# Optimization experiments

Measured on AMD Instinct MI355X. Metric: run time of the kernel, lower is better.

Reference implementation:

```python
import jax, jax.numpy as jnp
import numpy as np

D_MODEL = 256
N_HEADS = 8
D_FF = 1024
N_LAYERS = 6
INPUT_DIM = 2
EPS = 1e-5  # torch LayerNorm default


def _layer_norm(x, g, b):
    m = jnp.mean(x, axis=-1, keepdims=True)
    v = jnp.mean((x - m) ** 2, axis=-1, keepdims=True)
    return (x - m) / jnp.sqrt(v + EPS) * g + b


def setup_inputs() -> dict:
    key = jax.random.key(0)
    ks = jax.random.split(key, 8)
    f32 = jnp.float32

    def w(k, shape, fan_in):
        return jax.random.normal(k, shape, f32) * (1.0 / np.sqrt(fan_in))

    return {
        "x": jax.random.normal(ks[0], (8, 1024, INPUT_DIM), f32),
        "in_w": w(ks[1], (INPUT_DIM, D_MODEL), INPUT_DIM),
        "in_b": jnp.zeros((D_MODEL,), f32),
        "ln1_g": jnp.ones((D_MODEL,), f32),
        "ln1_b": jnp.zeros((D_MODEL,), f32),
        "qkv_w": w(ks[2], (D_MODEL, 3 * D_MODEL), D_MODEL),
        "qkv_b": jnp.zeros((3 * D_MODEL,), f32),
        "out_w": w(ks[3], (D_MODEL, D_MODEL), D_MODEL),
        "out_b": jnp.zeros((D_MODEL,), f32),
        "lna_g": jnp.ones((D_MODEL,), f32),
        "lna_b": jnp.zeros((D_MODEL,), f32),
        "ln2_g": jnp.ones((D_MODEL,), f32),
        "ln2_b": jnp.zeros((D_MODEL,), f32),
        "ff1_w": w(ks[4], (D_MODEL, D_FF), D_MODEL),
        "ff1_b": jnp.zeros((D_FF,), f32),
        "ff2_w": w(ks[5], (D_FF, D_MODEL), D_FF),
        "ff2_b": jnp.zeros((D_MODEL,), f32),
        "lnf_g": jnp.ones((D_MODEL,), f32),
        "lnf_b": jnp.zeros((D_MODEL,), f32),
    }


def reference(x, in_w, in_b, ln1_g, ln1_b, qkv_w, qkv_b, out_w, out_b,
              lna_g, lna_b, ln2_g, ln2_b, ff1_w, ff1_b, ff2_w, ff2_b,
              lnf_g, lnf_b):
    B, L, _ = x.shape
    dk = D_MODEL // N_HEADS
    scale = 1.0 / np.sqrt(dk)
    top_k = max(1, L // 4)

    # sinusoidal positional encoding [L, D]
    pos = jnp.arange(L, dtype=jnp.float32)[:, None]
    div = jnp.exp(jnp.arange(0, D_MODEL, 2, dtype=jnp.float32)
                  * (-np.log(10000.0) / D_MODEL))
    pe = jnp.zeros((L, D_MODEL), jnp.float32)
    pe = pe.at[:, 0::2].set(jnp.sin(pos * div))
    pe = pe.at[:, 1::2].set(jnp.cos(pos * div))

    h = x @ in_w + in_b + pe[None]  # [B, L, D]

    # VoformerEncoder reuses the SAME layer object -> shared weights, 6 passes
    for _ in range(N_LAYERS):
        # --- self-attention sublayer (pre-norm) ---
        s2 = _layer_norm(h, ln1_g, ln1_b)
        qkv = (s2 @ qkv_w + qkv_b).reshape(B, L, 3, N_HEADS, dk)
        q = qkv[:, :, 0].transpose(0, 2, 1, 3)  # [B, H, L, dk]
        k = qkv[:, :, 1].transpose(0, 2, 1, 3)
        v = qkv[:, :, 2].transpose(0, 2, 1, 3)

        scores = jnp.einsum('bhqd,bhkd->bhqk', q, k) * scale  # [B,H,L,L]
        # ProbSparse: keep only the per-row top-k scores
        thr = jax.lax.top_k(scores, top_k)[0][..., -1:]
        sparse = jnp.where(scores >= thr, scores, -jnp.inf)
        attn = jax.nn.softmax(sparse, axis=-1)
        o = jnp.einsum('bhqk,bhkd->bhqd', attn, v)
        o = o.transpose(0, 2, 1, 3).reshape(B, L, D_MODEL)
        o = o @ out_w + out_b
        # InformerAttention applies its own residual + LayerNorm
        attn_out = _layer_norm(o + s2, lna_g, lna_b)
        h = h + attn_out

        # --- FFN sublayer with Volatilite activation ---
        s2 = _layer_norm(h, ln2_g, ln2_b)
        f = s2 @ ff1_w + ff1_b  # [B, L, d_ff]
        mean_f = jnp.mean(f, axis=1, keepdims=True)
        vol = jnp.sqrt(jnp.mean((mean_f - f) ** 2, axis=1, keepdims=True))
        f = f * vol
        f = f @ ff2_w + ff2_b
        h = h + f

    return _layer_norm(h, lnf_g, lnf_b)
```

## Files before the change

kernel.cpp:

```cpp
#include <hip/hip_runtime.h>
#include <math.h>

#define D_MODEL 256
#define NH 8
#define DFF 1024
#define NLAYERS 6
#define B_ 8
#define L_ 1024
#define NR (B_*L_)
#define TOPK 256
#define LNEPS 1e-5f

typedef __attribute__((ext_vector_type(8))) short bf16x8;
typedef __attribute__((ext_vector_type(4))) float f32x4;

__device__ __forceinline__ float wsum(float v){
  #pragma unroll
  for(int o=32;o>0;o>>=1) v += __shfl_xor(v,o,64);
  return v;
}
__device__ __forceinline__ short f2bf(float x){
  unsigned u = __float_as_uint(x);
  u += 0x7fffu + ((u>>16)&1u);
  return (short)(u>>16);
}
__device__ __forceinline__ float bf2f(short s){
  return __uint_as_float(((unsigned)(unsigned short)s)<<16);
}
__device__ __forceinline__ int sortkey(unsigned u){
  return (u & 0x8000u) ? (int)(u ^ 0xFFFFu) : (int)(u | 0x8000u);
}
__device__ __forceinline__ float kinvf(int k){
  unsigned u = (k & 0x8000) ? ((unsigned)k ^ 0x8000u) : ((unsigned)k ^ 0xFFFFu);
  return __uint_as_float(u << 16);
}
__device__ __forceinline__ void g2l(const short* g, short* l){
  __builtin_amdgcn_global_load_lds(
      (const __attribute__((address_space(1))) unsigned int*)g,
      (__attribute__((address_space(3))) unsigned int*)l,
      16, 0, 0);
}

__global__ __launch_bounds__(256) void embed_kernel(
    const float* __restrict__ x, const float* __restrict__ in_w,
    const float* __restrict__ in_b, float* __restrict__ h)
{
  int tid = blockIdx.x*256 + threadIdx.x;
  int n  = tid >> 6;
  int d0 = (tid & 63) << 2;
  int l  = n & (L_-1);
  float x0 = x[2*n], x1 = x[2*n+1];
  const float kf = -0.07195578415606394f;
  float pe[4];
  #pragma unroll
  for(int ii=0; ii<2; ++ii){
    int i = (d0>>1) + ii;
    float dv  = expf((float)i * kf);
    float ang = (float)l * dv;
    pe[2*ii]   = sinf(ang);
    pe[2*ii+1] = cosf(ang);
  }
  float4 w0 = *(const float4*)(in_w + d0);
  float4 w1 = *(const float4*)(in_w + D_MODEL + d0);
  float4 bb = *(const float4*)(in_b + d0);
  float4 o;
  o.x = x0*w0.x + x1*w1.x + bb.x + pe[0];
  o.y = x0*w0.y + x1*w1.y + bb.y + pe[1];
  o.z = x0*w0.z + x1*w1.z + bb.z + pe[2];
  o.w = x0*w0.w + x1*w1.w + bb.w + pe[3];
  *(float4*)(h + (size_t)n*D_MODEL + d0) = o;
}

__global__ __launch_bounds__(256) void wcvt(
    const float* __restrict__ W, short* __restrict__ WT, int N, int kshift)
{
  int idx = blockIdx.x*256 + threadIdx.x;
  int K = 1<<kshift;
  if (idx >= N*K) return;
  int n = idx >> kshift, k = idx & (K-1);
  WT[idx] = f2bf(W[(size_t)k*N + n]);
}

template<int OM>
__global__ __launch_bounds__(256) void ln_kernel(
    const float* __restrict__ in, const float* __restrict__ g,
    const float* __restrict__ b, float* __restrict__ out,
    short* __restrict__ outb)
{
  int wave = threadIdx.x >> 6, lane = threadIdx.x & 63;
  int row = blockIdx.x*4 + wave;
  float4 v = ((const float4*)(in + (size_t)row*D_MODEL))[lane];
  float s  = v.x+v.y+v.z+v.w;
  float sq = v.x*v.x+v.y*v.y+v.z*v.z+v.w*v.w;
  s = wsum(s); sq = wsum(sq);
  float mean = s*(1.f/D_MODEL);
  float var  = sq*(1.f/D_MODEL) - mean*mean;
  float rstd = 1.f/sqrtf(var + LNEPS);
  float4 gv = ((const float4*)g)[lane];
  float4 bv = ((const float4*)b)[lane];
  float4 o;
  o.x = (v.x-mean)*rstd*gv.x + bv.x;
  o.y = (v.y-mean)*rstd*gv.y + bv.y;
  o.z = (v.z-mean)*rstd*gv.z + bv.z;
  o.w = (v.w-mean)*rstd*gv.w + bv.w;
  if (OM == 0){
    ((float4*)(out + (size_t)row*D_MODEL))[lane] = o;
  }
  if (OM == 2){
    short4 s4; s4.x=f2bf(o.x); s4.y=f2bf(o.y); s4.z=f2bf(o.z); s4.w=f2bf(o.w);
    *(short4*)(outb + (size_t)row*D_MODEL + lane*4) = s4;
  }
}

__global__ __launch_bounds__(256) void lnln_kernel(
    const float* __restrict__ tb,
    const float* __restrict__ ga, const float* __restrict__ ba,
    const float* __restrict__ g2, const float* __restrict__ b2,
    float* __restrict__ h, short* __restrict__ s2b)
{
  int wave = threadIdx.x >> 6, lane = threadIdx.x & 63;
  int row = blockIdx.x*4 + wave;
  float4 v = ((const float4*)(tb + (size_t)row*D_MODEL))[lane];
  float s  = v.x+v.y+v.z+v.w;
  float sq = v.x*v.x+v.y*v.y+v.z*v.z+v.w*v.w;
  s = wsum(s); sq = wsum(sq);
  float mean = s*(1.f/D_MODEL);
  float var  = sq*(1.f/D_MODEL) - mean*mean;
  float rstd = 1.f/sqrtf(var + LNEPS);
  float4 gv = ((const float4*)ga)[lane];
  float4 bv = ((const float4*)ba)[lane];
  float4* hp = (float4*)(h + (size_t)row*D_MODEL) + lane;
  float4 hv = *hp;
  float4 hn;
  hn.x = hv.x + (v.x-mean)*rstd*gv.x + bv.x;
  hn.y = hv.y + (v.y-mean)*rstd*gv.y + bv.y;
  hn.z = hv.z + (v.z-mean)*rstd*gv.z + bv.z;
  hn.w = hv.w + (v.w-mean)*rstd*gv.w + bv.w;
  *hp = hn;
  float s2  = hn.x+hn.y+hn.z+hn.w;
  float sq2 = hn.x*hn.x+hn.y*hn.y+hn.z*hn.z+hn.w*hn.w;
  s2 = wsum(s2); sq2 = wsum(sq2);
  float m2 = s2*(1.f/D_MODEL);
  float v2 = sq2*(1.f/D_MODEL) - m2*m2;
  float r2 = 1.f/sqrtf(v2 + LNEPS);
  float4 g2v = ((const float4*)g2)[lane];
  float4 b2v = ((const float4*)b2)[lane];
  short4 s4;
  s4.x = f2bf((hn.x-m2)*r2*g2v.x + b2v.x);
  s4.y = f2bf((hn.y-m2)*r2*g2v.y + b2v.y);
  s4.z = f2bf((hn.z-m2)*r2*g2v.z + b2v.z);
  s4.w = f2bf((hn.w-m2)*r2*g2v.w + b2v.w);
  *(short4*)(s2b + (size_t)row*D_MODEL + lane*4) = s4;
}

template<int MODE>
__global__ __launch_bounds__(256) void mfma_gemm(
    const short* __restrict__ A, const short* __restrict__ BT,
    const float* __restrict__ bias, const short* __restrict__ residb,
    float* __restrict__ Cf, short* __restrict__ Cb, short* __restrict__ Vt,
    int N, int K)
{
  __shared__ __align__(16) short As[128*32];
  __shared__ __align__(16) short Bs[64*32];
  const int t = threadIdx.x, wv = t>>6, lane = t&63;
  const int r16 = lane&15, quad = lane>>4;
  const int m0 = blockIdx.y*128, n0 = blockIdx.x*64;
  const int ia0 = wv*128 + lane, ia1 = ia0 + 64;
  const int ib  = wv*64 + lane;
  const short* Ab = A  + (size_t)m0*K;
  const short* Bb = BT + (size_t)n0*K;
  const f32x4 z = {0.f,0.f,0.f,0.f};
  f32x4 acc[2][4];
  #pragma unroll
  for (int i=0;i<2;++i)
    #pragma unroll
    for (int j=0;j<4;++j) acc[i][j] = z;

  for (int k0 = 0; k0 < K; k0 += 32){
    __syncthreads();
    g2l(Ab + (size_t)(ia0>>2)*K + k0 + (ia0&3)*8, As + ia0*8);
    g2l(Ab + (size_t)(ia1>>2)*K + k0 + (ia1&3)*8, As + ia1*8);
    g2l(Bb + (size_t)(ib>>2)*K  + k0 + (ib&3)*8,  Bs + ib*8);
    __syncthreads();
    bf16x8 af0 = *(const bf16x8*)(As + ((wv*32      + r16)*32 + quad*8));
    bf16x8 af1 = *(const bf16x8*)(As + ((wv*32 + 16 + r16)*32 + quad*8));
    bf16x8 bf[4];
    #pragma unroll
    for (int ct=0; ct<4; ++ct)
      bf[ct] = *(const bf16x8*)(Bs + ((ct*16 + r16)*32 + quad*8));
    #pragma unroll
    for (int ct=0; ct<4; ++ct){
      acc[0][ct] = __builtin_amdgcn_mfma_f32_16x16x32_bf16(af0, bf[ct], acc[0][ct], 0,0,0);
      acc[1][ct] = __builtin_amdgcn_mfma_f32_16x16x32_bf16(af1, bf[ct], acc[1][ct], 0,0,0);
    }
  }

  #pragma unroll
  for (int rt=0; rt<2; ++rt){
    const int mb = m0 + wv*32 + rt*16 + quad*4;
    #pragma unroll
    for (int ct=0; ct<4; ++ct){
      const int n = n0 + ct*16 + r16;
      const float bv = bias[n];
      if (MODE == 0){
        if (n < 512){
          int region = n>>8, hh = (n>>5)&7, d = n&31;
          #pragma unroll
          for (int r=0;r<4;++r){
            int l = mb + r;
            size_t base = (((size_t)(region*64 + (l>>10)*8 + hh))*1024 + (l&1023))*32 + d;
            Cb[base] = f2bf(acc[rt][ct][r] + bv);
          }
        } else {
          int dv = n - 512, hh = dv>>5, d = dv&31;
          int b = mb>>10, lloc = mb&1023;
          size_t base = (((size_t)(b*8 + hh))*32 + d)*1024 + lloc;
          short4 s4;
          s4.x = f2bf(acc[rt][ct][0] + bv); s4.y = f2bf(acc[rt][ct][1] + bv);
          s4.z = f2bf(acc[rt][ct][2] + bv); s4.w = f2bf(acc[rt][ct][3] + bv);
          *(short4*)(Vt + base) = s4;
        }
      } else {
        #pragma unroll
        for (int r=0;r<4;++r){
          size_t off = (size_t)(mb + r)*N + n;
          float c = acc[rt][ct][r] + bv;
          if (MODE == 1) Cf[off] = c + bf2f(residb[off]);
          if (MODE == 2) Cb[off] = f2bf(c);
          if (MODE == 3) Cf[off] += c;
        }
      }
    }
  }
}

__global__ __launch_bounds__(256,4) void attn_mfma(
    const short* __restrict__ qkbf, const short* __restrict__ vT,
    short* __restrict__ ob)
{
  __shared__ __align__(16) short sc16[16*1024];
  __shared__ float linv[16];
  const int t = threadIdx.x, wv = t>>6, lane = t&63;
  const int r16 = lane&15, quad = lane>>4;
  const int blk = blockIdx.x;
  const int bh = (blk & 7)*8 + ((blk>>3)&7);
  const int qt = blk >> 6;

  bf16x8 aq = *(const bf16x8*)(qkbf + ((size_t)bh*1024 + qt*16 + r16)*32 + quad*8);
  const short* kb = qkbf + (size_t)(64 + bh)*1024*32;

  bf16x8 bk[16];
  #pragma unroll
  for (int tt=0; tt<16; ++tt)
    bk[tt] = *(const bf16x8*)(kb + (size_t)(wv*256 + tt*16 + r16)*32 + quad*8);
  #pragma unroll
  for (int tt=0; tt<16; ++tt){
    f32x4 c = {0.f,0.f,0.f,0.f};
    c = __builtin_amdgcn_mfma_f32_16x16x32_bf16(aq, bk[tt], c, 0, 0, 0);
    const int pos = wv*256 + ((tt ^ quad)<<4) + r16;
    #pragma unroll
    for (int r=0;r<4;++r)
      sc16[(quad*4+r)*1024 + pos] = f2bf(c[r]);
  }
  __syncthreads();

  const float SC2 = 0.25500529485087056f;
  const int sw = wv << 4;
  short* prow = sc16 + ((2*lane) ^ sw);
  for (int rp=0; rp<2; ++rp){
    const int ra = wv*4 + rp*2;
    short* pa = prow + ra*1024;
    short* pb = pa + 1024;
    unsigned wa[8], wb[8];
    #pragma unroll
    for (int i=0;i<8;++i){
      wa[i] = *(const unsigned*)(pa + i*128);
      wb[i] = *(const unsigned*)(pb + i*128);
    }
    int ka[16], kb2[16];
    #pragma unroll
    for (int i=0;i<8;++i){
      ka[2*i]    = sortkey(wa[i] & 0xFFFFu);
      ka[2*i+1]  = sortkey(wa[i] >> 16);
      kb2[2*i]   = sortkey(wb[i] & 0xFFFFu);
      kb2[2*i+1] = sortkey(wb[i] >> 16);
    }
    int mxa = ka[0], mxb = kb2[0];
    #pragma unroll
    for (int i=1;i<16;++i){
      mxa = (ka[i]  > mxa) ? ka[i]  : mxa;
      mxb = (kb2[i] > mxb) ? kb2[i] : mxb;
    }
    #pragma unroll
    for (int o=32;o>0;o>>=1){
      int sa = __shfl_xor(mxa, o, 64); mxa = (sa > mxa) ? sa : mxa;
      int sb = __shfl_xor(mxb, o, 64); mxb = (sb > mxb) ? sb : mxb;
    }
    int loA=0, hiA=mxa+1, loB=0, hiB=mxb+1;
    while (hiA-loA > 1 || hiB-loB > 1){
      int midA = (loA+hiA)>>1, midB = (loB+hiB)>>1;
      int cA=0, cB=0;
      #pragma unroll
      for (int i=0;i<16;++i){
        cA += (int)__popcll(__ballot(ka[i]  >= midA));
        cB += (int)__popcll(__ballot(kb2[i] >= midB));
      }
      if (cA >= TOPK) loA = midA; else hiA = midA;
      if (cB >= TOPK) loB = midB; else hiB = midB;
    }
    const float thrA = kinvf(loA), thrB = kinvf(loB);
    const float nmA = -kinvf(mxa)*SC2, nmB = -kinvf(mxb)*SC2;
    float suma = 0.f, sumb = 0.f;
    unsigned pka[8], pkb[8];
    #pragma unroll
    for (int i=0;i<8;++i){
      float a0 = __uint_as_float(wa[i] << 16);
      float a1 = __uint_as_float(wa[i] & 0xFFFF0000u);
      float b0 = __uint_as_float(wb[i] << 16);
      float b1 = __uint_as_float(wb[i] & 0xFFFF0000u);
      float ea0 = (a0 >= thrA) ? exp2f(fmaf(a0, SC2, nmA)) : 0.f;
      float ea1 = (a1 >= thrA) ? exp2f(fmaf(a1, SC2, nmA)) : 0.f;
      float eb0 = (b0 >= thrB) ? exp2f(fmaf(b0, SC2, nmB)) : 0.f;
      float eb1 = (b1 >= thrB) ? exp2f(fmaf(b1, SC2, nmB)) : 0.f;
      suma += ea0 + ea1; sumb += eb0 + eb1;
      pka[i] = (unsigned)(unsigned short)f2bf(ea0) | ((unsigned)(unsigned short)f2bf(ea1) << 16);
      pkb[i] = (unsigned)(unsigned short)f2bf(eb0) | ((unsigned)(unsigned short)f2bf(eb1) << 16);
    }
    suma = wsum(suma); sumb = wsum(sumb);
    if (lane == 0){ linv[ra] = 1.f/suma; linv[ra+1] = 1.f/sumb; }
    #pragma unroll
    for (int i=0;i<8;++i){
      *(unsigned*)(pa + i*128) = pka[i];
      *(unsigned*)(pb + i*128) = pkb[i];
    }
  }
  __syncthreads();

  const short* vb = vT + (size_t)bh*32*1024;
  bf16x8 bvv[16];
  #pragma unroll
  for (int tt=0; tt<8; ++tt){
    int k0 = wv*256 + tt*32;
    #pragma unroll
    for (int n=0;n<2;++n)
      bvv[tt*2+n] = *(const bf16x8*)(vb + (size_t)(n*16 + r16)*1024 + k0 + quad*8);
  }
  const int sA = ((r16>>2)&3) << 4;
  f32x4 oa0 = {0.f,0.f,0.f,0.f}, oa1 = {0.f,0.f,0.f,0.f};
  #pragma unroll
  for (int tt=0; tt<8; ++tt){
    int k0 = wv*256 + tt*32;
    bf16x8 af = *(const bf16x8*)(sc16 + r16*1024 + ((k0 + quad*8) ^ sA));
    oa0 = __builtin_amdgcn_mfma_f32_16x16x32_bf16(af, bvv[tt*2+0], oa0, 0, 0, 0);
    oa1 = __builtin_amdgcn_mfma_f32_16x16x32_bf16(af, bvv[tt*2+1], oa1, 0, 0, 0);
  }
  __syncthreads();
  float* po = (float*)sc16;
  #pragma unroll
  for (int r=0;r<4;++r){
    po[wv*512 + (quad*4+r)*32 +      r16] = oa0[r];
    po[wv*512 + (quad*4+r)*32 + 16 + r16] = oa1[r];
  }
  __syncthreads();
  int e = t*2;
  float v0 = po[e]   + po[512+e]   + po[1024+e]   + po[1536+e];
  float v1 = po[e+1] + po[512+e+1] + po[1024+e+1] + po[1536+e+1];
  int q = e>>5, d = e&31;
  const float inv = linv[q];
  int b = bh>>3, hh = bh&7;
  size_t off = ((size_t)(b*1024 + qt*16 + q))*256 + hh*32 + d;
  short2 s2o; s2o.x = f2bf(v0*inv); s2o.y = f2bf(v1*inv);
  *(short2*)(ob + off) = s2o;
}

__global__ __launch_bounds__(512) void vol_scale(short* __restrict__ f)
{
  __shared__ float ps[8][64], pq[8][64], vs[64];
  int b = blockIdx.x >> 4, cb = blockIdx.x & 15;
  int cl = threadIdx.x & 63, sl = threadIdx.x >> 6;
  int col = cb*64 + cl;
  short* fb = f + (size_t)b*L_*DFF + col;
  float s = 0.f, sq = 0.f;
  for (int l = sl*128; l < sl*128+128; ++l){
    float v = bf2f(fb[(size_t)l*DFF]);
    s += v; sq += v*v;
  }
  ps[sl][cl] = s; pq[sl][cl] = sq;
  __syncthreads();
  if (threadIdx.x < 64){
    float st=0.f, qt=0.f;
    #pragma unroll
    for (int i=0;i<8;++i){ st += ps[i][cl]; qt += pq[i][cl]; }
    float mean = st*(1.f/L_);
    float var  = qt*(1.f/L_) - mean*mean;
    vs[cl] = sqrtf(fmaxf(var, 0.f));
  }
  __syncthreads();
  float vv = vs[cl];
  for (int l = sl*128; l < sl*128+128; ++l){
    size_t o = (size_t)l*DFF;
    fb[o] = f2bf(bf2f(fb[o]) * vv);
  }
}

extern "C" void kernel_launch(void* const* d_in, const int* in_sizes, int n_in,
                              void* d_out, int out_size, void* d_ws, size_t ws_size,
                              hipStream_t stream) {
  const float* x     = (const float*)d_in[0];
  const float* in_w  = (const float*)d_in[1];
  const float* in_b  = (const float*)d_in[2];
  const float* ln1_g = (const float*)d_in[3];
  const float* ln1_b = (const float*)d_in[4];
  const float* qkv_w = (const float*)d_in[5];
  const float* qkv_b = (const float*)d_in[6];
  const float* out_w = (const float*)d_in[7];
  const float* out_b = (const float*)d_in[8];
  const float* lna_g = (const float*)d_in[9];
  const float* lna_b = (const float*)d_in[10];
  const float* ln2_g = (const float*)d_in[11];
  const float* ln2_b = (const float*)d_in[12];
  const float* ff1_w = (const float*)d_in[13];
  const float* ff1_b = (const float*)d_in[14];
  const float* ff2_w = (const float*)d_in[15];
  const float* ff2_b = (const float*)d_in[16];
  const float* lnf_g = (const float*)d_in[17];
  const float* lnf_b = (const float*)d_in[18];
  float* out = (float*)d_out;

  char* ws = (char*)d_ws;
  float* h     = (float*)(ws);
  short* s2b   = (short*)(ws + (size_t)( 8<<20));
  short* qkbf  = (short*)(ws + (size_t)(12<<20));
  short* vTb   = (short*)(ws + (size_t)(20<<20));
  short* ob_b  = (short*)(ws + (size_t)(24<<20));
  short* f     = (short*)(ws + (size_t)(12<<20));
  float* tb    = (float*)(ws + (size_t)(28<<20));
  short* qkvwT = (short*)(ws + (size_t)(36<<20));
  short* outwT = (short*)(ws + (size_t)(36<<20) + 393216);
  short* ff1wT = (short*)(ws + (size_t)(36<<20) + 393216 + 131072);
  short* ff2wT = (short*)(ws + (size_t)(36<<20) + 393216 + 131072 + 524288);

  embed_kernel<<<NR*64/256, 256, 0, stream>>>(x, in_w, in_b, h);
  wcvt<<< 768, 256, 0, stream>>>(qkv_w, qkvwT,  768, 8);
  wcvt<<< 256, 256, 0, stream>>>(out_w, outwT,  256, 8);
  wcvt<<<1024, 256, 0, stream>>>(ff1_w, ff1wT, 1024, 8);
  wcvt<<<1024, 256, 0, stream>>>(ff2_w, ff2wT,  256, 10);

  for (int layer = 0; layer < NLAYERS; ++layer){
    ln_kernel<2><<<NR/4, 256, 0, stream>>>(h, ln1_g, ln1_b, nullptr, s2b);
    {
      dim3 g(768/64, NR/128);
      mfma_gemm<0><<<g, 256, 0, stream>>>(s2b, qkvwT, qkv_b, nullptr,
                                          nullptr, qkbf, vTb, 768, 256);
    }
    attn_mfma<<<64*64, 256, 0, stream>>>(qkbf, vTb, ob_b);
    {
      dim3 g(256/64, NR/128);
      mfma_gemm<1><<<g, 256, 0, stream>>>(ob_b, outwT, out_b, s2b,
                                          tb, nullptr, nullptr, 256, 256);
    }
    lnln_kernel<<<NR/4, 256, 0, stream>>>(tb, lna_g, lna_b, ln2_g, ln2_b, h, s2b);
    {
      dim3 g(1024/64, NR/128);
      mfma_gemm<2><<<g, 256, 0, stream>>>(s2b, ff1wT, ff1_b, nullptr,
                                          nullptr, f, nullptr, 1024, 256);
    }
    vol_scale<<<B_*16, 512, 0, stream>>>(f);
    {
      dim3 g(256/64, NR/128);
      mfma_gemm<3><<<g, 256, 0, stream>>>(f, ff2wT, ff2_b, nullptr,
                                          h, nullptr, nullptr, 256, 1024);
    }
  }
  ln_kernel<0><<<NR/4, 256, 0, stream>>>(h, lnf_g, lnf_b, out, nullptr);
}
```

Baseline: 1.282 ms.

## Slim attention kernel registers, bitwise float top-k search, packed bf16 conversions

Reworks the ProbSparse attention kernel to use fewer registers so it can run five blocks per CU. K and V fragments are now loaded in small groups instead of holding all 16 at once. Scores get a new LDS swizzle and are written with packed bf16 conversion. The top-k threshold is now a fixed 16-step bitwise search comparing floats directly, replacing the sort-key conversion, the row-max reduction and the data-dependent bisection. Softmax drops its max subtraction, which risks exp2 overflow on large scores. Row inverse sums stay in registers instead of LDS, and the other kernels use the packed float2-to-bf16 intrinsic for their bf16 stores.

```diff
diff --git a/kernel.cpp b/kernel.cpp
--- a/kernel.cpp
+++ b/kernel.cpp
@@ -1,4 +1,5 @@
 #include <hip/hip_runtime.h>
+#include <hip/hip_bf16.h>
 #include <math.h>
 
 #define D_MODEL 256
@@ -27,8 +28,10 @@
 __device__ __forceinline__ float bf2f(short s){
   return __uint_as_float(((unsigned)(unsigned short)s)<<16);
 }
-__device__ __forceinline__ int sortkey(unsigned u){
-  return (u & 0x8000u) ? (int)(u ^ 0xFFFFu) : (int)(u | 0x8000u);
+__device__ __forceinline__ unsigned pk2bf(float a, float b){
+  __hip_bfloat162 h = __float22bfloat162_rn(make_float2(a,b));
+  unsigned u; __builtin_memcpy(&u, &h, 4);
+  return u;
 }
 __device__ __forceinline__ float kinvf(int k){
   unsigned u = (k & 0x8000) ? ((unsigned)k ^ 0x8000u) : ((unsigned)k ^ 0xFFFFu);
@@ -107,8 +110,8 @@
     ((float4*)(out + (size_t)row*D_MODEL))[lane] = o;
   }
   if (OM == 2){
-    short4 s4; s4.x=f2bf(o.x); s4.y=f2bf(o.y); s4.z=f2bf(o.z); s4.w=f2bf(o.w);
-    *(short4*)(outb + (size_t)row*D_MODEL + lane*4) = s4;
+    uint2 pk; pk.x = pk2bf(o.x, o.y); pk.y = pk2bf(o.z, o.w);
+    *(uint2*)(outb + (size_t)row*D_MODEL + lane*4) = pk;
   }
 }
 
@@ -145,12 +148,10 @@
   float r2 = 1.f/sqrtf(v2 + LNEPS);
   float4 g2v = ((const float4*)g2)[lane];
   float4 b2v = ((const float4*)b2)[lane];
-  short4 s4;
-  s4.x = f2bf((hn.x-m2)*r2*g2v.x + b2v.x);
-  s4.y = f2bf((hn.y-m2)*r2*g2v.y + b2v.y);
-  s4.z = f2bf((hn.z-m2)*r2*g2v.z + b2v.z);
-  s4.w = f2bf((hn.w-m2)*r2*g2v.w + b2v.w);
-  *(short4*)(s2b + (size_t)row*D_MODEL + lane*4) = s4;
+  uint2 pk;
+  pk.x = pk2bf((hn.x-m2)*r2*g2v.x + b2v.x, (hn.y-m2)*r2*g2v.y + b2v.y);
+  pk.y = pk2bf((hn.z-m2)*r2*g2v.z + b2v.z, (hn.w-m2)*r2*g2v.w + b2v.w);
+  *(uint2*)(s2b + (size_t)row*D_MODEL + lane*4) = pk;
 }
 
 template<int MODE>
@@ -215,10 +216,10 @@
           int dv = n - 512, hh = dv>>5, d = dv&31;
           int b = mb>>10, lloc = mb&1023;
           size_t base = (((size_t)(b*8 + hh))*32 + d)*1024 + lloc;
-          short4 s4;
-          s4.x = f2bf(acc[rt][ct][0] + bv); s4.y = f2bf(acc[rt][ct][1] + bv);
-          s4.z = f2bf(acc[rt][ct][2] + bv); s4.w = f2bf(acc[rt][ct][3] + bv);
-          *(short4*)(Vt + base) = s4;
+          uint2 pk;
+          pk.x = pk2bf(acc[rt][ct][0] + bv, acc[rt][ct][1] + bv);
+          pk.y = pk2bf(acc[rt][ct][2] + bv, acc[rt][ct][3] + bv);
+          *(uint2*)(Vt + base) = pk;
         }
       } else {
         #pragma unroll
@@ -234,12 +235,11 @@
   }
 }
 
-__global__ __launch_bounds__(256,4) void attn_mfma(
+__global__ __launch_bounds__(256,5) void attn_mfma(
     const short* __restrict__ qkbf, const short* __restrict__ vT,
     short* __restrict__ ob)
 {
   __shared__ __align__(16) short sc16[16*1024];
-  __shared__ float linv[16];
   const int t = threadIdx.x, wv = t>>6, lane = t&63;
   const int r16 = lane&15, quad = lane>>4;
   const int blk = blockIdx.x;
@@ -248,111 +248,107 @@
 
   bf16x8 aq = *(const bf16x8*)(qkbf + ((size_t)bh*1024 + qt*16 + r16)*32 + quad*8);
   const short* kb = qkbf + (size_t)(64 + bh)*1024*32;
-
-  bf16x8 bk[16];
-  #pragma unroll
-  for (int tt=0; tt<16; ++tt)
-    bk[tt] = *(const bf16x8*)(kb + (size_t)(wv*256 + tt*16 + r16)*32 + quad*8);
-  #pragma unroll
-  for (int tt=0; tt<16; ++tt){
-    f32x4 c = {0.f,0.f,0.f,0.f};
-    c = __builtin_amdgcn_mfma_f32_16x16x32_bf16(aq, bk[tt], c, 0, 0, 0);
-    const int pos = wv*256 + ((tt ^ quad)<<4) + r16;
-    #pragma unroll
-    for (int r=0;r<4;++r)
-      sc16[(quad*4+r)*1024 + pos] = f2bf(c[r]);
+  short* p0 = sc16 + quad*4096;
+
+  #pragma unroll
+  for (int g=0; g<4; ++g){
+    bf16x8 bkb[4];
+    #pragma unroll
+    for (int j=0;j<4;++j)
+      bkb[j] = *(const bf16x8*)(kb + (size_t)(wv*256 + (g*4+j)*16 + r16)*32 + quad*8);
+    #pragma unroll
+    for (int j=0;j<4;++j){
+      f32x4 c = {0.f,0.f,0.f,0.f};
+      c = __builtin_amdgcn_mfma_f32_16x16x32_bf16(aq, bkb[j], c, 0, 0, 0);
+      const int keyq = (wv*256 + (g*4+j)*16 + r16) ^ ((quad&1)<<5);
+      unsigned u01 = pk2bf(c[0], c[1]);
+      unsigned u23 = pk2bf(c[2], c[3]);
+      p0[keyq]               = (short)u01;
+      p0[1024 + (keyq ^ 8)]  = (short)(u01>>16);
+      p0[2048 + (keyq ^ 16)] = (short)u23;
+      p0[3072 + (keyq ^ 24)] = (short)(u23>>16);
+    }
   }
   __syncthreads();
 
   const float SC2 = 0.25500529485087056f;
-  const int sw = wv << 4;
-  short* prow = sc16 + ((2*lane) ^ sw);
+  float iv0, iv1, iv2, iv3;
+  #pragma unroll
   for (int rp=0; rp<2; ++rp){
     const int ra = wv*4 + rp*2;
-    short* pa = prow + ra*1024;
-    short* pb = pa + 1024;
-    unsigned wa[8], wb[8];
+    const int sa = (ra&7)<<3;
+    short* pa = sc16 + ra*1024 + ((2*lane) ^ sa);
+    short* pb = sc16 + (ra+1)*1024 + (((2*lane) ^ sa) ^ 8);
+    float fa[16], fb[16];
     #pragma unroll
     for (int i=0;i<8;++i){
-      wa[i] = *(const unsigned*)(pa + i*128);
-      wb[i] = *(const unsigned*)(pb + i*128);
-    }
-    int ka[16], kb2[16];
-    #pragma unroll
-    for (int i=0;i<8;++i){
-      ka[2*i]    = sortkey(wa[i] & 0xFFFFu);
-      ka[2*i+1]  = sortkey(wa[i] >> 16);
-      kb2[2*i]   = sortkey(wb[i] & 0xFFFFu);
-      kb2[2*i+1] = sortkey(wb[i] >> 16);
-    }
-    int mxa = ka[0], mxb = kb2[0];
-    #pragma unroll
-    for (int i=1;i<16;++i){
-      mxa = (ka[i]  > mxa) ? ka[i]  : mxa;
-      mxb = (kb2[i] > mxb) ? kb2[i] : mxb;
-    }
-    #pragma unroll
-    for (int o=32;o>0;o>>=1){
-      int sa = __shfl_xor(mxa, o, 64); mxa = (sa > mxa) ? sa : mxa;
-      int sb = __shfl_xor(mxb, o, 64); mxb = (sb > mxb) ? sb : mxb;
-    }
-    int loA=0, hiA=mxa+1, loB=0, hiB=mxb+1;
-    while (hiA-loA > 1 || hiB-loB > 1){
-      int midA = (loA+hiA)>>1, midB = (loB+hiB)>>1;
-      int cA=0, cB=0;
+      unsigned wa = *(const unsigned*)(pa + i*128);
+      unsigned wb = *(const unsigned*)(pb + i*128);
+      fa[2*i]   = __uint_as_float(wa << 16);
+      fa[2*i+1] = __uint_as_float(wa & 0xFFFF0000u);
+      fb[2*i]   = __uint_as_float(wb << 16);
+      fb[2*i+1] = __uint_as_float(wb & 0xFFFF0000u);
+    }
+    int loA = 0, loB = 0;
+    #pragma unroll
+    for (int bit = 15; bit >= 0; --bit){
+      const int mA = loA | (1<<bit);
+      const int mB = loB | (1<<bit);
+      const float tA = kinvf(mA);
+      const float tB = kinvf(mB);
+      int cA = 0, cB = 0;
       #pragma unroll
       for (int i=0;i<16;++i){
-        cA += (int)__popcll(__ballot(ka[i]  >= midA));
-        cB += (int)__popcll(__ballot(kb2[i] >= midB));
+        cA += (int)__popcll(__ballot(fa[i] >= tA));
+        cB += (int)__popcll(__ballot(fb[i] >= tB));
       }
-      if (cA >= TOPK) loA = midA; else hiA = midA;
-      if (cB >= TOPK) loB = midB; else hiB = midB;
+      if (cA >= TOPK) loA = mA;
+      if (cB >= TOPK) loB = mB;
     }
     const float thrA = kinvf(loA), thrB = kinvf(loB);
-    const float nmA = -kinvf(mxa)*SC2, nmB = -kinvf(mxb)*SC2;
     float suma = 0.f, sumb = 0.f;
     unsigned pka[8], pkb[8];
     #pragma unroll
     for (int i=0;i<8;++i){
-      float a0 = __uint_as_float(wa[i] << 16);
-      float a1 = __uint_as_float(wa[i] & 0xFFFF0000u);
-      float b0 = __uint_as_float(wb[i] << 16);
-      float b1 = __uint_as_float(wb[i] & 0xFFFF0000u);
-      float ea0 = (a0 >= thrA) ? exp2f(fmaf(a0, SC2, nmA)) : 0.f;
-      float ea1 = (a1 >= thrA) ? exp2f(fmaf(a1, SC2, nmA)) : 0.f;
-      float eb0 = (b0 >= thrB) ? exp2f(fmaf(b0, SC2, nmB)) : 0.f;
-      float eb1 = (b1 >= thrB) ? exp2f(fmaf(b1, SC2, nmB)) : 0.f;
+      float ea0 = (fa[2*i]   >= thrA) ? exp2f(fa[2*i]  *SC2) : 0.f;
+      float ea1 = (fa[2*i+1] >= thrA) ? exp2f(fa[2*i+1]*SC2) : 0.f;
+      float eb0 = (fb[2*i]   >= thrB) ? exp2f(fb[2*i]  *SC2) : 0.f;
+      float eb1 = (fb[2*i+1] >= thrB) ? exp2f(fb[2*i+1]*SC2) : 0.f;
       suma += ea0 + ea1; sumb += eb0 + eb1;
-      pka[i] = (unsigned)(unsigned short)f2bf(ea0) | ((unsigned)(unsigned short)f2bf(ea1) << 16);
-      pkb[i] = (unsigned)(unsigned short)f2bf(eb0) | ((unsigned)(unsigned short)f2bf(eb1) << 16);
+      pka[i] = pk2bf(ea0, ea1);
+      pkb[i] = pk2bf(eb0, eb1);
     }
     suma = wsum(suma); sumb = wsum(sumb);
-    if (lane == 0){ linv[ra] = 1.f/suma; linv[ra+1] = 1.f/sumb; }
+    if (rp == 0){ iv0 = 1.f/suma; iv1 = 1.f/sumb; }
+    else        { iv2 = 1.f/suma; iv3 = 1.f/sumb; }
     #pragma unroll
     for (int i=0;i<8;++i){
       *(unsigned*)(pa + i*128) = pka[i];
       *(unsigned*)(pb + i*128) = pkb[i];
     }
   }
+  const float invq = (quad==0)?iv0 : (quad==1)?iv1 : (quad==2)?iv2 : iv3;
   __syncthreads();
 
   const short* vb = vT + (size_t)bh*32*1024;
-  bf16x8 bvv[16];
-  #pragma unroll
-  for (int tt=0; tt<8; ++tt){
-    int k0 = wv*256 + tt*32;
-    #pragma unroll
-    for (int n=0;n<2;++n)
-      bvv[tt*2+n] = *(const bf16x8*)(vb + (size_t)(n*16 + r16)*1024 + k0 + quad*8);
-  }
-  const int sA = ((r16>>2)&3) << 4;
+  const int sA = (r16&7) << 3;
   f32x4 oa0 = {0.f,0.f,0.f,0.f}, oa1 = {0.f,0.f,0.f,0.f};
   #pragma unroll
-  for (int tt=0; tt<8; ++tt){
-    int k0 = wv*256 + tt*32;
-    bf16x8 af = *(const bf16x8*)(sc16 + r16*1024 + ((k0 + quad*8) ^ sA));
-    oa0 = __builtin_amdgcn_mfma_f32_16x16x32_bf16(af, bvv[tt*2+0], oa0, 0, 0, 0);
-    oa1 = __builtin_amdgcn_mfma_f32_16x16x32_bf16(af, bvv[tt*2+1], oa1, 0, 0, 0);
+  for (int g=0; g<4; ++g){
+    bf16x8 bvb[4];
+    #pragma unroll
+    for (int j=0;j<2;++j){
+      int k0 = wv*256 + (g*2+j)*32;
+      bvb[j*2+0] = *(const bf16x8*)(vb + (size_t)(     r16)*1024 + k0 + quad*8);
+      bvb[j*2+1] = *(const bf16x8*)(vb + (size_t)(16 + r16)*1024 + k0 + quad*8);
+    }
+    #pragma unroll
+    for (int j=0;j<2;++j){
+      int k0 = wv*256 + (g*2+j)*32;
+      bf16x8 af = *(const bf16x8*)(sc16 + r16*1024 + ((k0 + quad*8) ^ sA));
+      oa0 = __builtin_amdgcn_mfma_f32_16x16x32_bf16(af, bvb[j*2+0], oa0, 0, 0, 0);
+      oa1 = __builtin_amdgcn_mfma_f32_16x16x32_bf16(af, bvb[j*2+1], oa1, 0, 0, 0);
+    }
   }
   __syncthreads();
   float* po = (float*)sc16;
@@ -366,11 +362,9 @@
   float v0 = po[e]   + po[512+e]   + po[1024+e]   + po[1536+e];
   float v1 = po[e+1] + po[512+e+1] + po[1024+e+1] + po[1536+e+1];
   int q = e>>5, d = e&31;
-  const float inv = linv[q];
   int b = bh>>3, hh = bh&7;
   size_t off = ((size_t)(b*1024 + qt*16 + q))*256 + hh*32 + d;
-  short2 s2o; s2o.x = f2bf(v0*inv); s2o.y = f2bf(v1*inv);
-  *(short2*)(ob + off) = s2o;
+  *(unsigned*)(ob + off) = pk2bf(v0*invq, v1*invq);
 }
 
 __global__ __launch_bounds__(512) void vol_scale(short* __restrict__ f)
```

Measured after the change: 1.273 ms. Within noise of the previous version (-0.7%).
